# Optimization experiments

Hardware: AMD Instinct MI355X
Metric: run time of the kernel (lower is better)

Reference implementation:

```python
import jax, jax.numpy as jnp
import numpy as np

EPS = 1e-09


def setup_inputs() -> dict:
    key = jax.random.key(0)
    k1, k2 = jax.random.split(key)
    vocab_size, embed_dim = 128000, 1024
    psi = jax.random.normal(k1, (embed_dim,), dtype=jnp.float32)
    vocab_reps = jax.random.normal(k2, (vocab_size, embed_dim), dtype=jnp.float32)
    return {"psi": psi, "vocab_reps": vocab_reps, "top_k": 5}


def reference(psi, vocab_reps, top_k):
    # Normalize query state: psi / (||psi|| + eps)
    psi_norm = psi / (jnp.linalg.norm(psi) + EPS)
    # Normalize every vocab row: [V, D] / ([V, 1] + eps)
    vocab_norms = vocab_reps / (jnp.linalg.norm(vocab_reps, axis=1, keepdims=True) + EPS)
    # Cosine similarities via GEVM: [V]
    similarities = vocab_norms @ psi_norm
    top_scores, top_indices = jax.lax.top_k(similarities, top_k)
    return top_scores, top_indices
```

## Files before the change

### kernel.cpp

```cpp
#include <hip/hip_runtime.h>
#include <math.h>
#include <limits.h>

#define EPS  1e-9f
#define TOPK 5

typedef float v4f __attribute__((ext_vector_type(4)));

__device__ __forceinline__ bool better(float av, int ai, float bv, int bi) {
    return (av > bv) || (av == bv && ai < bi);
}

__device__ __forceinline__ void insert_top(float sv[TOPK], int si[TOPK], float v, int idx) {
    if (!better(v, idx, sv[TOPK - 1], si[TOPK - 1])) return;
    sv[TOPK - 1] = v; si[TOPK - 1] = idx;
#pragma unroll
    for (int j = TOPK - 1; j > 0; --j) {
        if (better(sv[j], si[j], sv[j - 1], si[j - 1])) {
            float tv = sv[j]; sv[j] = sv[j - 1]; sv[j - 1] = tv;
            int   ti = si[j]; si[j] = si[j - 1]; si[j - 1] = ti;
        }
    }
}

__device__ __forceinline__ float dot4(v4f a, v4f b) {
    return a.x * b.x + a.y * b.y + a.z * b.z + a.w * b.w;
}

__global__ __launch_bounds__(256) void sim_top_kernel(const v4f* __restrict__ vocab,
                                                      const v4f* __restrict__ psi4,
                                                      float* __restrict__ cand_v,
                                                      int* __restrict__ cand_i,
                                                      int V) {
    __shared__ float wvs[4 * TOPK];
    __shared__ int   wis[4 * TOPK];
    const int tid  = threadIdx.x;
    const int lane = tid & 63;
    const int wave = tid >> 6;
    const int wavesPerBlock = blockDim.x >> 6;
    const int gwave  = blockIdx.x * wavesPerBlock + wave;
    const int nwaves = gridDim.x * wavesPerBlock;

    const v4f p0 = psi4[lane];
    const v4f p1 = psi4[64 + lane];
    const v4f p2 = psi4[128 + lane];
    const v4f p3 = psi4[192 + lane];

    float ps = dot4(p0, p0) + dot4(p1, p1) + dot4(p2, p2) + dot4(p3, p3);
    for (int off = 32; off > 0; off >>= 1) ps += __shfl_xor(ps, off);
    const float scale = 1.0f / (sqrtf(ps) + EPS);

    float tv[TOPK]; int ti[TOPK];
#pragma unroll
    for (int j = 0; j < TOPK; ++j) { tv[j] = -INFINITY; ti[j] = INT_MAX; }

    const int NP = V >> 1;
    for (int p = gwave; p < NP; p += nwaves) {
        const v4f* ra = vocab + (size_t)(2 * p) * 256;
        const v4f* rb = ra + 256;
        v4f a0 = __builtin_nontemporal_load(ra + lane);
        v4f a1 = __builtin_nontemporal_load(ra + 64 + lane);
        v4f a2 = __builtin_nontemporal_load(ra + 128 + lane);
        v4f a3 = __builtin_nontemporal_load(ra + 192 + lane);
        v4f b0 = __builtin_nontemporal_load(rb + lane);
        v4f b1 = __builtin_nontemporal_load(rb + 64 + lane);
        v4f b2 = __builtin_nontemporal_load(rb + 128 + lane);
        v4f b3 = __builtin_nontemporal_load(rb + 192 + lane);

        float dotA = dot4(a0, p0) + dot4(a1, p1) + dot4(a2, p2) + dot4(a3, p3);
        float nrmA = dot4(a0, a0) + dot4(a1, a1) + dot4(a2, a2) + dot4(a3, a3);
        float dotB = dot4(b0, p0) + dot4(b1, p1) + dot4(b2, p2) + dot4(b3, p3);
        float nrmB = dot4(b0, b0) + dot4(b1, b1) + dot4(b2, b2) + dot4(b3, b3);

        for (int off = 32; off > 0; off >>= 1) {
            dotA += __shfl_xor(dotA, off);
            nrmA += __shfl_xor(nrmA, off);
            dotB += __shfl_xor(dotB, off);
            nrmB += __shfl_xor(nrmB, off);
        }
        if (lane == 0) {
            insert_top(tv, ti, dotA * scale / (sqrtf(nrmA) + EPS), 2 * p);
            insert_top(tv, ti, dotB * scale / (sqrtf(nrmB) + EPS), 2 * p + 1);
        }
    }

    if ((V & 1) && gwave == 0) {
        const int row = V - 1;
        const v4f* ra = vocab + (size_t)row * 256;
        v4f a0 = ra[lane], a1 = ra[64 + lane], a2 = ra[128 + lane], a3 = ra[192 + lane];
        float dotA = dot4(a0, p0) + dot4(a1, p1) + dot4(a2, p2) + dot4(a3, p3);
        float nrmA = dot4(a0, a0) + dot4(a1, a1) + dot4(a2, a2) + dot4(a3, a3);
        for (int off = 32; off > 0; off >>= 1) {
            dotA += __shfl_xor(dotA, off);
            nrmA += __shfl_xor(nrmA, off);
        }
        if (lane == 0) insert_top(tv, ti, dotA * scale / (sqrtf(nrmA) + EPS), row);
    }

    if (lane == 0) {
#pragma unroll
        for (int j = 0; j < TOPK; ++j) { wvs[wave * TOPK + j] = tv[j]; wis[wave * TOPK + j] = ti[j]; }
    }
    __syncthreads();
    if (tid == 0) {
        float bv[TOPK]; int bi[TOPK];
#pragma unroll
        for (int j = 0; j < TOPK; ++j) { bv[j] = -INFINITY; bi[j] = INT_MAX; }
        for (int e = 0; e < wavesPerBlock * TOPK; ++e) insert_top(bv, bi, wvs[e], wis[e]);
#pragma unroll
        for (int j = 0; j < TOPK; ++j) {
            cand_v[blockIdx.x * TOPK + j] = bv[j];
            cand_i[blockIdx.x * TOPK + j] = bi[j];
        }
    }
}

__global__ __launch_bounds__(1024) void topk_reduce_kernel(const float* __restrict__ cand_v,
                                                           const int* __restrict__ cand_i,
                                                           int NC, int K,
                                                           float* __restrict__ out) {
    __shared__ float wvs[16 * TOPK];
    __shared__ int   wis[16 * TOPK];
    const int tid = threadIdx.x;
    const int lane = tid & 63, wave = tid >> 6;
    const int nwaves = blockDim.x >> 6;

    float sv[TOPK]; int si[TOPK];
#pragma unroll
    for (int j = 0; j < TOPK; ++j) { sv[j] = -INFINITY; si[j] = INT_MAX; }

    for (int i = tid; i < NC; i += blockDim.x) insert_top(sv, si, cand_v[i], cand_i[i]);

    for (int step = 1; step < 64; step <<= 1) {
        float ov[TOPK]; int oi[TOPK];
#pragma unroll
        for (int j = 0; j < TOPK; ++j) {
            ov[j] = __shfl_xor(sv[j], step);
            oi[j] = __shfl_xor(si[j], step);
        }
#pragma unroll
        for (int j = 0; j < TOPK; ++j) insert_top(sv, si, ov[j], oi[j]);
    }

    if (lane == 0) {
#pragma unroll
        for (int j = 0; j < TOPK; ++j) { wvs[wave * TOPK + j] = sv[j]; wis[wave * TOPK + j] = si[j]; }
    }
    __syncthreads();
    if (tid == 0) {
        float bv[TOPK]; int bi[TOPK];
#pragma unroll
        for (int j = 0; j < TOPK; ++j) { bv[j] = -INFINITY; bi[j] = INT_MAX; }
        for (int e = 0; e < nwaves * TOPK; ++e) insert_top(bv, bi, wvs[e], wis[e]);
        for (int k = 0; k < K && k < TOPK; ++k) {
            out[k]     = bv[k];
            out[K + k] = (float)bi[k];
        }
    }
}

extern "C" void kernel_launch(void* const* d_in, const int* in_sizes, int n_in,
                              void* d_out, int out_size, void* d_ws, size_t ws_size,
                              hipStream_t stream) {
    const float* psi   = (const float*)d_in[0];
    const float* vocab = (const float*)d_in[1];
    const int D = in_sizes[0];
    const int V = in_sizes[1] / D;
    const int K = out_size / 2;
    (void)D;

    const int blocks = 2000;
    const int NC = blocks * TOPK;

    float* cand_v = (float*)d_ws;
    int*   cand_i = (int*)((float*)d_ws + NC);

    sim_top_kernel<<<blocks, 256, 0, stream>>>((const v4f*)vocab, (const v4f*)psi,
                                               cand_v, cand_i, V);

    topk_reduce_kernel<<<1, 1024, 0, stream>>>(cand_v, cand_i, NC, K, (float*)d_out);
}
```

Before: 113.7 us.

## Fuse final top-k reduction into main kernel via last-block atomic counter

Removes the separate single-block top-k reduce kernel. Each block bumps a global atomic counter after writing its candidates, and the last block to finish reduces all candidates and writes the output. This saves a kernel launch and the gap between kernels, but adds a hipMemsetAsync to reset the counter and leaves the final reduction on a 256-thread block instead of 1024 threads.

```diff
diff --git a/kernel.cpp b/kernel.cpp
--- a/kernel.cpp
+++ b/kernel.cpp
@@ -27,19 +27,25 @@
     return a.x * b.x + a.y * b.y + a.z * b.z + a.w * b.w;
 }
 
+#define NTLOAD(p) __builtin_nontemporal_load(p)
+
 __global__ __launch_bounds__(256) void sim_top_kernel(const v4f* __restrict__ vocab,
                                                       const v4f* __restrict__ psi4,
                                                       float* __restrict__ cand_v,
                                                       int* __restrict__ cand_i,
-                                                      int V) {
+                                                      unsigned int* __restrict__ counter,
+                                                      int V, int K,
+                                                      float* __restrict__ out) {
     __shared__ float wvs[4 * TOPK];
     __shared__ int   wis[4 * TOPK];
+    __shared__ int   s_last;
     const int tid  = threadIdx.x;
     const int lane = tid & 63;
     const int wave = tid >> 6;
     const int wavesPerBlock = blockDim.x >> 6;
     const int gwave  = blockIdx.x * wavesPerBlock + wave;
     const int nwaves = gridDim.x * wavesPerBlock;
+    const int NC = gridDim.x * TOPK;
 
     const v4f p0 = psi4[lane];
     const v4f p1 = psi4[64 + lane];
@@ -57,15 +63,14 @@
     const int NP = V >> 1;
     for (int p = gwave; p < NP; p += nwaves) {
         const v4f* ra = vocab + (size_t)(2 * p) * 256;
-        const v4f* rb = ra + 256;
-        v4f a0 = __builtin_nontemporal_load(ra + lane);
-        v4f a1 = __builtin_nontemporal_load(ra + 64 + lane);
-        v4f a2 = __builtin_nontemporal_load(ra + 128 + lane);
-        v4f a3 = __builtin_nontemporal_load(ra + 192 + lane);
-        v4f b0 = __builtin_nontemporal_load(rb + lane);
-        v4f b1 = __builtin_nontemporal_load(rb + 64 + lane);
-        v4f b2 = __builtin_nontemporal_load(rb + 128 + lane);
-        v4f b3 = __builtin_nontemporal_load(rb + 192 + lane);
+        v4f a0 = NTLOAD(ra + lane);
+        v4f a1 = NTLOAD(ra + 64 + lane);
+        v4f a2 = NTLOAD(ra + 128 + lane);
+        v4f a3 = NTLOAD(ra + 192 + lane);
+        v4f b0 = NTLOAD(ra + 256 + lane);
+        v4f b1 = NTLOAD(ra + 320 + lane);
+        v4f b2 = NTLOAD(ra + 384 + lane);
+        v4f b3 = NTLOAD(ra + 448 + lane);
 
         float dotA = dot4(a0, p0) + dot4(a1, p1) + dot4(a2, p2) + dot4(a3, p3);
         float nrmA = dot4(a0, a0) + dot4(a1, a1) + dot4(a2, a2) + dot4(a3, a3);
@@ -112,49 +117,45 @@
             cand_v[blockIdx.x * TOPK + j] = bv[j];
             cand_i[blockIdx.x * TOPK + j] = bi[j];
         }
-    }
-}
-
-__global__ __launch_bounds__(1024) void topk_reduce_kernel(const float* __restrict__ cand_v,
-                                                           const int* __restrict__ cand_i,
-                                                           int NC, int K,
-                                                           float* __restrict__ out) {
-    __shared__ float wvs[16 * TOPK];
-    __shared__ int   wis[16 * TOPK];
-    const int tid = threadIdx.x;
-    const int lane = tid & 63, wave = tid >> 6;
-    const int nwaves = blockDim.x >> 6;
-
-    float sv[TOPK]; int si[TOPK];
-#pragma unroll
-    for (int j = 0; j < TOPK; ++j) { sv[j] = -INFINITY; si[j] = INT_MAX; }
-
-    for (int i = tid; i < NC; i += blockDim.x) insert_top(sv, si, cand_v[i], cand_i[i]);
-
-    for (int step = 1; step < 64; step <<= 1) {
-        float ov[TOPK]; int oi[TOPK];
-#pragma unroll
-        for (int j = 0; j < TOPK; ++j) {
-            ov[j] = __shfl_xor(sv[j], step);
-            oi[j] = __shfl_xor(si[j], step);
-        }
-#pragma unroll
-        for (int j = 0; j < TOPK; ++j) insert_top(sv, si, ov[j], oi[j]);
-    }
-
-    if (lane == 0) {
-#pragma unroll
-        for (int j = 0; j < TOPK; ++j) { wvs[wave * TOPK + j] = sv[j]; wis[wave * TOPK + j] = si[j]; }
+        __threadfence();
+        unsigned int prev = atomicAdd(counter, 1u);
+        s_last = (prev == (unsigned int)(gridDim.x - 1)) ? 1 : 0;
     }
     __syncthreads();
-    if (tid == 0) {
-        float bv[TOPK]; int bi[TOPK];
+
+    if (s_last) {
+        __threadfence();
+        float sv[TOPK]; int si[TOPK];
 #pragma unroll
-        for (int j = 0; j < TOPK; ++j) { bv[j] = -INFINITY; bi[j] = INT_MAX; }
-        for (int e = 0; e < nwaves * TOPK; ++e) insert_top(bv, bi, wvs[e], wis[e]);
-        for (int k = 0; k < K && k < TOPK; ++k) {
-            out[k]     = bv[k];
-            out[K + k] = (float)bi[k];
+        for (int j = 0; j < TOPK; ++j) { sv[j] = -INFINITY; si[j] = INT_MAX; }
+        for (int i = tid; i < NC; i += blockDim.x)
+            insert_top(sv, si, cand_v[i], cand_i[i]);
+
+        for (int step = 1; step < 64; step <<= 1) {
+            float ov[TOPK]; int oi[TOPK];
+#pragma unroll
+            for (int j = 0; j < TOPK; ++j) {
+                ov[j] = __shfl_xor(sv[j], step);
+                oi[j] = __shfl_xor(si[j], step);
+            }
+#pragma unroll
+            for (int j = 0; j < TOPK; ++j) insert_top(sv, si, ov[j], oi[j]);
+        }
+
+        if (lane == 0) {
+#pragma unroll
+            for (int j = 0; j < TOPK; ++j) { wvs[wave * TOPK + j] = sv[j]; wis[wave * TOPK + j] = si[j]; }
+        }
+        __syncthreads();
+        if (tid == 0) {
+            float bv[TOPK]; int bi[TOPK];
+#pragma unroll
+            for (int j = 0; j < TOPK; ++j) { bv[j] = -INFINITY; bi[j] = INT_MAX; }
+            for (int e = 0; e < wavesPerBlock * TOPK; ++e) insert_top(bv, bi, wvs[e], wis[e]);
+            for (int k = 0; k < K && k < TOPK; ++k) {
+                out[k]     = bv[k];
+                out[K + k] = (float)bi[k];
+            }
         }
     }
 }
@@ -172,11 +173,13 @@
     const int blocks = 2000;
     const int NC = blocks * TOPK;
 
-    float* cand_v = (float*)d_ws;
-    int*   cand_i = (int*)((float*)d_ws + NC);
+    float*        cand_v  = (float*)d_ws;
+    int*          cand_i  = (int*)((float*)d_ws + NC);
+    unsigned int* counter = (unsigned int*)(cand_i + NC);
+
+    hipMemsetAsync(counter, 0, sizeof(unsigned int), stream);
 
     sim_top_kernel<<<blocks, 256, 0, stream>>>((const v4f*)vocab, (const v4f*)psi,
-                                               cand_v, cand_i, V);
-
-    topk_reduce_kernel<<<1, 1024, 0, stream>>>(cand_v, cand_i, NC, K, (float*)d_out);
+                                               cand_v, cand_i, counter, V, K,
+                                               (float*)d_out);
 }
```

Result: slower. 181.4 us (+59.5%).
